# Performance work log

Hardware: AMD Instinct MI355X
Metric: run time of the kernel (lower is better)

The kernel has to match this reference:

```python
import jax, jax.numpy as jnp
import numpy as np

B, T_RED, C = 16, 512, 512
MAX_DUR = 16


def setup_inputs() -> dict:
    key = jax.random.key(0)
    rng = np.random.default_rng(0)
    durs = np.zeros((B, T_RED), dtype=np.int32)
    for b in range(B):
        nv = int(rng.integers(T_RED // 2, T_RED + 1))
        durs[b, :nv] = rng.integers(1, MAX_DUR + 1, size=nv)
    target_T = durs.sum(axis=1).astype(np.int32)
    pooled_x = jax.random.normal(key, (B, T_RED, C), dtype=jnp.float32)
    return {
        "pooled_x": pooled_x,
        "durations": jnp.asarray(durs),
        "target_T": jnp.asarray(target_T),
    }


def reference(pooled_x, durations, target_T):
    # pooled_x: [B, T_red, C]; durations: [B, T_red] int (0 = pad); target_T: [B]
    Bv, T_red, Cv = pooled_x.shape
    max_len = int(jnp.max(target_T))  # concrete (eager) like the torch .item()

    # torch: valid_durs = durations[b][durations[b] > 0]; feats = pooled_x[b, :num_valid]
    # -> stably compact nonzero durations to the front; pair with leading features.
    order = jnp.argsort(jnp.where(durations > 0, 0, 1), axis=1, stable=True)
    d = jnp.take_along_axis(durations, order, axis=1)            # [B, T_red]
    csum = jnp.cumsum(d, axis=1)                                 # [B, T_red]

    t = jnp.arange(max_len, dtype=csum.dtype)                    # [max_len]
    # repeat_interleave inverse: output frame t belongs to segment
    # s = searchsorted(csum, t, 'right')  (csum[s-1] <= t < csum[s])
    seg = jax.vmap(lambda c: jnp.searchsorted(c, t, side="right"))(csum)  # [B, max_len]
    seg = jnp.minimum(seg, T_red - 1)

    total = csum[:, -1]                                          # len(repeat_interleave result)
    curr_len = jnp.minimum(total, target_T)                      # [B]
    valid = t[None, :] < curr_len[:, None]                       # [B, max_len]

    gathered = jnp.take_along_axis(pooled_x, seg[:, :, None], axis=1)  # [B, max_len, C]
    x_restored = jnp.where(valid[:, :, None], gathered, jnp.zeros((), pooled_x.dtype))
    new_mask = jnp.where(valid, 0, 1).astype(jnp.int32)          # 0 = valid, 1 = padded
    return x_restored, new_mask
```

## Files before the change

kernel.cpp:

```cpp
#include <hip/hip_runtime.h>

#define B_DIM 16
#define T_RED 512
#define C_DIM 512
#define ROWS_PER_BLK 16
#define NXCD 8
#define MAX_ML_PAD 20480

typedef float vfloat4 __attribute__((ext_vector_type(4)));

__device__ int g_ls[B_DIM * MAX_ML_PAD];

__device__ inline int block_scan256(int v, int* wsum ) {
    const int lane = threadIdx.x & 63;
    const int wid  = threadIdx.x >> 6;
    int s = v;
    #pragma unroll
    for (int off = 1; off < 64; off <<= 1) {
        int n = __shfl_up(s, off, 64);
        if (lane >= off) s += n;
    }
    if (lane == 63) wsum[wid] = s;
    __syncthreads();
    int add = 0;
    #pragma unroll
    for (int w = 0; w < 4; ++w)
        if (w < wid) add += wsum[w];
    int out = s + add;
    __syncthreads();
    return out;
}

__global__ __launch_bounds__(256) void build_ls(
        const int2* __restrict__ dur2,
        float* __restrict__ out_mask,
        int max_len, int ml_pad) {
    const int b   = blockIdx.x;
    const int tid = threadIdx.x;

    __shared__ int dcomp[T_RED];
    __shared__ int wsum[4];

    const int2 dd = dur2[b * (T_RED / 2) + tid];
    const int d0 = dd.x, d1 = dd.y;
    const int f0 = (d0 > 0) ? 1 : 0;
    const int f1 = (d1 > 0) ? 1 : 0;

    const int S1 = block_scan256(f0 + f1, wsum);
    const int excl = S1 - f0 - f1;
    dcomp[2 * tid]     = 0;
    dcomp[2 * tid + 1] = 0;
    __syncthreads();
    if (f0) dcomp[excl] = d0;
    if (f1) dcomp[excl + f0] = d1;
    __syncthreads();

    const int c0 = dcomp[2 * tid];
    const int c1 = dcomp[2 * tid + 1];
    const int S2 = block_scan256(c0 + c1, wsum);
    const int total = wsum[0] + wsum[1] + wsum[2] + wsum[3];

    int* lsb = g_ls + (size_t)b * ml_pad;

    const int st0 = S2 - c1 - c0;
    for (int k = 0; k < c0; ++k) lsb[st0 + k] = 2 * tid;
    const int st1 = S2 - c1;
    for (int k = 0; k < c1; ++k) lsb[st1 + k] = 2 * tid + 1;

    for (int t = total + tid; t < ml_pad; t += 256) lsb[t] = -1;

    float* mb = out_mask + (size_t)b * max_len;
    for (int t = tid; t < max_len; t += 256) mb[t] = (t < total) ? 0.0f : 1.0f;
}

__global__ __launch_bounds__(256) void gather_rows(
        const vfloat4* __restrict__ x4,
        vfloat4* __restrict__ out4,
        int max_len, int ml_pad, int blk_per_b) {
    const int nwg  = gridDim.x;
    const int orig = blockIdx.x;
    const int q = nwg / NXCD, r = nwg % NXCD;
    const int xcd = orig % NXCD, idx = orig / NXCD;
    const int wg  = (xcd < r ? xcd * (q + 1) : r * (q + 1) + (xcd - r) * q) + idx;

    const int b    = wg / blk_per_b;
    const int base = (wg % blk_per_b) * ROWS_PER_BLK;
    const int tid  = threadIdx.x;
    const int c4   = tid & 127;
    const int half = tid >> 7;

    const int* lsb = g_ls + (size_t)b * ml_pad + base;
    int srcs[8];
    #pragma unroll
    for (int p = 0; p < 8; ++p) srcs[p] = lsb[2 * p + half];

    const vfloat4* xb = x4 + (size_t)b * T_RED * (C_DIM / 4);
    vfloat4 v[8];
    #pragma unroll
    for (int p = 0; p < 8; ++p) {
        const int sc = (srcs[p] >= 0) ? srcs[p] : 0;
        v[p] = xb[(size_t)sc * (C_DIM / 4) + c4];
    }

    vfloat4* ob = out4 + ((size_t)b * max_len + base) * (C_DIM / 4);
    #pragma unroll
    for (int p = 0; p < 8; ++p) {
        const int lr = 2 * p + half;
        const int t  = base + lr;
        if (t < max_len) {
            const vfloat4 vv = (srcs[p] >= 0) ? v[p] : (vfloat4)(0.0f);
            ob[(size_t)lr * (C_DIM / 4) + c4] = vv;
        }
    }
}

__global__ __launch_bounds__(256) void scatter_fused(
        const vfloat4* __restrict__ x4,
        const int2* __restrict__ dur2,
        vfloat4* __restrict__ out4,
        float* __restrict__ out_mask,
        int max_len) {
    const int b    = blockIdx.y;
    const int base = blockIdx.x * ROWS_PER_BLK;
    const int tid  = threadIdx.x;

    __shared__ int dcomp[T_RED];
    __shared__ int csum[T_RED];
    __shared__ int wsum[4];
    __shared__ int ls[ROWS_PER_BLK];

    const int2 dd = dur2[b * (T_RED / 2) + tid];
    const int d0 = dd.x, d1 = dd.y;
    const int f0 = (d0 > 0) ? 1 : 0;
    const int f1 = (d1 > 0) ? 1 : 0;

    const int S1 = block_scan256(f0 + f1, wsum);
    const int excl = S1 - f0 - f1;
    dcomp[2 * tid]     = 0;
    dcomp[2 * tid + 1] = 0;
    __syncthreads();
    if (f0) dcomp[excl] = d0;
    if (f1) dcomp[excl + f0] = d1;
    __syncthreads();

    const int c0 = dcomp[2 * tid];
    const int c1 = dcomp[2 * tid + 1];
    const int S2 = block_scan256(c0 + c1, wsum);
    csum[2 * tid]     = S2 - c1;
    csum[2 * tid + 1] = S2;
    __syncthreads();

    const int total = csum[T_RED - 1];

    if (tid < ROWS_PER_BLK) {
        const int t = base + tid;
        int src = -1;
        if (t < max_len && t < total) {
            int idx = 0;
            #pragma unroll
            for (int w = 256; w >= 1; w >>= 1) {
                const int cand = idx + w;
                if (cand <= T_RED && csum[cand - 1] <= t) idx = cand;
            }
            const int seg = (idx < T_RED - 1) ? idx : (T_RED - 1);
            src = b * T_RED + seg;
        }
        if (t < max_len) {
            ls[tid] = src;
            out_mask[(size_t)b * max_len + t] = (src >= 0) ? 0.0f : 1.0f;
        }
    }
    __syncthreads();

    const int c4   = tid & 127;
    const int half = tid >> 7;
    #pragma unroll
    for (int p = 0; p < 8; ++p) {
        const int lr = 2 * p + half;
        const int t  = base + lr;
        if (t < max_len) {
            const int s = ls[lr];
            vfloat4 v = (vfloat4)(0.0f);
            if (s >= 0) v = x4[(size_t)s * (C_DIM / 4) + c4];
            out4[((size_t)b * max_len + t) * (C_DIM / 4) + c4] = v;
        }
    }
}

extern "C" void kernel_launch(void* const* d_in, const int* in_sizes, int n_in,
                              void* d_out, int out_size, void* d_ws, size_t ws_size,
                              hipStream_t stream) {
    const float* pooled_x  = (const float*)d_in[0];
    const int*   durations = (const int*)d_in[1];

    const int max_len = out_size / (B_DIM * (C_DIM + 1));
    const int ml_pad  = (max_len + ROWS_PER_BLK - 1) & ~(ROWS_PER_BLK - 1);

    float* out_x    = (float*)d_out;
    float* out_mask = out_x + (size_t)B_DIM * max_len * C_DIM;

    if (ml_pad <= MAX_ML_PAD) {
        build_ls<<<dim3(B_DIM), dim3(256), 0, stream>>>(
            (const int2*)durations, out_mask, max_len, ml_pad);

        const int blk_per_b = ml_pad / ROWS_PER_BLK;
        gather_rows<<<dim3(blk_per_b * B_DIM), dim3(256), 0, stream>>>(
            (const vfloat4*)pooled_x, (vfloat4*)out_x, max_len, ml_pad, blk_per_b);
    } else {
        dim3 grid((max_len + ROWS_PER_BLK - 1) / ROWS_PER_BLK, B_DIM);
        scatter_fused<<<grid, dim3(256), 0, stream>>>(
            (const vfloat4*)pooled_x, (const int2*)durations,
            (vfloat4*)out_x, out_mask, max_len);
    }
}
```

Baseline: 157.5 us.

## Replace 16-row gather blocks with one-float4-per-thread elementwise gather

New measurement: 169.8 us. 1.08x slower.

```diff
diff --git a/kernel.cpp b/kernel.cpp
--- a/kernel.cpp
+++ b/kernel.cpp
@@ -73,45 +73,30 @@
     for (int t = tid; t < max_len; t += 256) mb[t] = (t < total) ? 0.0f : 1.0f;
 }
 
-__global__ __launch_bounds__(256) void gather_rows(
+__global__ __launch_bounds__(256) void gather_elem(
         const vfloat4* __restrict__ x4,
         vfloat4* __restrict__ out4,
-        int max_len, int ml_pad, int blk_per_b) {
+        int max_len, int ml_pad) {
+    const int b = blockIdx.y;
+
     const int nwg  = gridDim.x;
     const int orig = blockIdx.x;
     const int q = nwg / NXCD, r = nwg % NXCD;
     const int xcd = orig % NXCD, idx = orig / NXCD;
-    const int wg  = (xcd < r ? xcd * (q + 1) : r * (q + 1) + (xcd - r) * q) + idx;
-
-    const int b    = wg / blk_per_b;
-    const int base = (wg % blk_per_b) * ROWS_PER_BLK;
-    const int tid  = threadIdx.x;
-    const int c4   = tid & 127;
-    const int half = tid >> 7;
-
-    const int* lsb = g_ls + (size_t)b * ml_pad + base;
-    int srcs[8];
-    #pragma unroll
-    for (int p = 0; p < 8; ++p) srcs[p] = lsb[2 * p + half];
-
-    const vfloat4* xb = x4 + (size_t)b * T_RED * (C_DIM / 4);
-    vfloat4 v[8];
-    #pragma unroll
-    for (int p = 0; p < 8; ++p) {
-        const int sc = (srcs[p] >= 0) ? srcs[p] : 0;
-        v[p] = xb[(size_t)sc * (C_DIM / 4) + c4];
-    }
-
-    vfloat4* ob = out4 + ((size_t)b * max_len + base) * (C_DIM / 4);
-    #pragma unroll
-    for (int p = 0; p < 8; ++p) {
-        const int lr = 2 * p + half;
-        const int t  = base + lr;
-        if (t < max_len) {
-            const vfloat4 vv = (srcs[p] >= 0) ? v[p] : (vfloat4)(0.0f);
-            ob[(size_t)lr * (C_DIM / 4) + c4] = vv;
-        }
-    }
+    const int bx  = (xcd < r ? xcd * (q + 1) : r * (q + 1) + (xcd - r) * q) + idx;
+
+    const int flat = bx * 256 + (int)threadIdx.x;
+    const int t    = flat >> 7;
+    const int c4   = flat & 127;
+    if (t >= max_len) return;
+
+    const int s = g_ls[b * ml_pad + t];
+
+    vfloat4 v = (vfloat4)(0.0f);
+    if (s >= 0)
+        v = x4[((size_t)b * T_RED + s) * (C_DIM / 4) + c4];
+
+    out4[((size_t)b * max_len + t) * (C_DIM / 4) + c4] = v;
 }
 
 __global__ __launch_bounds__(256) void scatter_fused(
@@ -203,9 +188,10 @@
         build_ls<<<dim3(B_DIM), dim3(256), 0, stream>>>(
             (const int2*)durations, out_mask, max_len, ml_pad);
 
-        const int blk_per_b = ml_pad / ROWS_PER_BLK;
-        gather_rows<<<dim3(blk_per_b * B_DIM), dim3(256), 0, stream>>>(
-            (const vfloat4*)pooled_x, (vfloat4*)out_x, max_len, ml_pad, blk_per_b);
+        const int f4_per_b = max_len * (C_DIM / 4);
+        const int nbx = (f4_per_b + 255) / 256;
+        gather_elem<<<dim3(nbx, B_DIM), dim3(256), 0, stream>>>(
+            (const vfloat4*)pooled_x, (vfloat4*)out_x, max_len, ml_pad);
     } else {
         dim3 grid((max_len + ROWS_PER_BLK - 1) / ROWS_PER_BLK, B_DIM);
         scatter_fused<<<grid, dim3(256), 0, stream>>>(
```
